# Performance work log

Hardware: AMD Instinct MI355X
Metric: run time of the kernel (lower is better)

The kernel has to match this reference:

```python
import jax, jax.numpy as jnp
import numpy as np

B, S, D = 4, 2048, 1024
NEG = -1e10

def setup_inputs() -> dict:
    key = jax.random.key(0)
    ks = jax.random.split(key, 8)
    scale = 1.0 / np.sqrt(D)
    return {
        "hidden_states": jax.random.normal(ks[0], (B, S, D), jnp.float32),
        "mask": jax.random.randint(ks[1], (B, S), 0, 2, jnp.int32),
        "Wq": jax.random.normal(ks[2], (D, D), jnp.float32) * scale,
        "bq": jnp.zeros((D,), jnp.float32),
        "Wk": jax.random.normal(ks[3], (D, D), jnp.float32) * scale,
        "bk": jnp.zeros((D,), jnp.float32),
        "Wv": jax.random.normal(ks[4], (D, D), jnp.float32) * scale,
        "bv": jnp.zeros((D,), jnp.float32),
        "Wo": jax.random.normal(ks[5], (D, D), jnp.float32) * scale,
        "bo": jnp.zeros((D,), jnp.float32),
    }

def reference(hidden_states, mask, Wq, bq, Wk, bk, Wv, bv, Wo, bo):
    # torch Linear: y = x @ W.T + b
    q = jnp.einsum('bsd,ed->bse', hidden_states, Wq) + bq
    k = jnp.einsum('bsd,ed->bse', hidden_states, Wk) + bk
    v = jnp.einsum('bsd,ed->bse', hidden_states, Wv) + bv
    inv_sqrt_d = jnp.asarray(int(hidden_states.shape[-1]) ** (-0.5), hidden_states.dtype)
    weight = jnp.einsum('bqd,bkd->bqk', q, k) * inv_sqrt_d  # [B,S,S]
    # mask viewed as [B,1,S]: key-padding mask broadcast over query dim
    m = mask.reshape(mask.shape[0], 1, mask.shape[1])
    weight = jnp.where(m == 0, jnp.asarray(NEG, weight.dtype), weight)
    a = jax.nn.softmax(weight, axis=-1)
    hid = jnp.einsum('bqk,bkd->bqd', a, v)
    hid_o = jnp.einsum('bsd,ed->bse', hid, Wo) + bo
    return hidden_states + hid_o  # residual=True
```

## Files before the change

### kernel.cpp

```cpp
#include <hip/hip_runtime.h>
#include <stdint.h>


typedef __attribute__((ext_vector_type(8))) short bf16x8;
typedef __attribute__((ext_vector_type(4))) float f32x4;

typedef __attribute__((address_space(3))) void lds_void_t;
typedef __attribute__((address_space(1))) const void glb_void_t;

__device__ __forceinline__ ushort f2bf(float f) {
  uint32_t u = __float_as_uint(f);
  u += 0x7FFF + ((u >> 16) & 1);
  return (ushort)(u >> 16);
}
__device__ __forceinline__ float bf2f(ushort u) {
  return __uint_as_float(((uint32_t)u) << 16);
}

__global__ __launch_bounds__(256) void convert_all(
    const float* __restrict__ X, const float* __restrict__ Wq,
    const float* __restrict__ Wk, const float* __restrict__ Wv,
    const float* __restrict__ Wo, const float* __restrict__ bq,
    const float* __restrict__ bk, const float* __restrict__ bv,
    ushort* __restrict__ Xb, ushort* __restrict__ Wqkvb,
    ushort* __restrict__ Wob, float* __restrict__ bqkv) {
  if (blockIdx.x >= 12288) {
#pragma unroll
    for (int u = 0; u < 3; ++u) {
      int base = (u * 256 + threadIdx.x) * 4;
      float4 v = (base < 1024)   ? *(const float4*)(bq + base)
               : (base < 2048)   ? *(const float4*)(bk + base - 1024)
                                 : *(const float4*)(bv + base - 2048);
      *(float4*)(bqkv + base) = v;
    }
    return;
  }
  int64_t o4 = ((int64_t)blockIdx.x * blockDim.x + threadIdx.x) * 4;
  const float* s; ushort* d; int64_t doff, soff;
  if (o4 < 8388608)        { s = X;  d = Xb;    doff = o4;            soff = o4; }
  else if (o4 < 9437184)   { s = Wq; d = Wqkvb; doff = o4 - 8388608;  soff = o4 - 8388608; }
  else if (o4 < 10485760)  { s = Wk; d = Wqkvb; doff = o4 - 8388608;  soff = o4 - 9437184; }
  else if (o4 < 11534336)  { s = Wv; d = Wqkvb; doff = o4 - 8388608;  soff = o4 - 10485760; }
  else                     { s = Wo; d = Wob;   doff = o4 - 11534336; soff = o4 - 11534336; }
  float4 v = *(const float4*)(s + soff);
  ushort4 o;
  o.x = f2bf(v.x); o.y = f2bf(v.y); o.z = f2bf(v.z); o.w = f2bf(v.w);
  *(ushort4*)(d + doff) = o;
}

#define BM 128
#define BKT 64

template <int MODE, int BNV>
__global__ __launch_bounds__(256) void gemm_bt(
    const ushort* __restrict__ Ag, const ushort* __restrict__ Bg,
    void* __restrict__ Og, const float* __restrict__ bias,
    const float* __restrict__ resid, ushort* __restrict__ Vt,
    const int* __restrict__ maskg, float* __restrict__ rowsum,
    int M, int N, int K, int lda, int ldb, int ldo,
    long long sAz, long long sBz, long long sOz, float scale) {
  constexpr int NFR = BNV / 32;
  __shared__ ushort LDSu[BM * BKT + BNV * BKT];
  ushort* const As = LDSu;
  ushort* const Bs = LDSu + BM * BKT;
  __shared__ int redn[4];

  const int z = blockIdx.z;
  const ushort* A = Ag + (int64_t)z * sAz;
  const ushort* B = Bg + (int64_t)z * sBz;

  const int tilesN = N / BNV;
  const int tm = blockIdx.x / tilesN;
  const int tn = blockIdx.x % tilesN;
  const int tid = threadIdx.x;
  const int wid = tid >> 6;
  const int lane = tid & 63;
  const int lr = lane & 15;
  const int kq = lane >> 4;
  const int wr = (wid >> 1) * 64;
  const int wc = (wid & 1) * (BNV / 2);

  if constexpr (MODE == 6) {
    const int4* mrow = (const int4*)(maskg + z * 2048);
    int4 ma = mrow[tid * 2];
    int4 mb = mrow[tid * 2 + 1];
    int cnt = (ma.x == 0) + (ma.y == 0) + (ma.z == 0) + (ma.w == 0) +
              (mb.x == 0) + (mb.y == 0) + (mb.z == 0) + (mb.w == 0);
#pragma unroll
    for (int off = 1; off < 64; off <<= 1) cnt += __shfl_xor(cnt, off);
    if (lane == 0) redn[wid] = cnt;
  }

  f32x4 acc[4][NFR];
#pragma unroll
  for (int m = 0; m < 4; ++m)
#pragma unroll
    for (int n = 0; n < NFR; ++n) acc[m][n] = (f32x4){0.f, 0.f, 0.f, 0.f};

  const int64_t abase = (int64_t)tm * BM;
  const int64_t bbase = (int64_t)tn * BNV;

  for (int kt = 0; kt < K; kt += BKT) {
    if (kt) __syncthreads();
#pragma unroll
    for (int r = 0; r < 4; ++r) {
      int idx = r * 256 + tid;
      int row = idx >> 3, slot = idx & 7;
      int sslot = slot ^ (row & 7);
      const ushort* ga = A + (abase + row) * lda + kt + sslot * 8;
      ushort* la = &As[(r * 256 + wid * 64) * 8];
      __builtin_amdgcn_global_load_lds((glb_void_t*)ga, (lds_void_t*)la, 16, 0, 0);
    }
#pragma unroll
    for (int r = 0; r < BNV / 32; ++r) {
      int idx = r * 256 + tid;
      int row = idx >> 3, slot = idx & 7;
      int sslot = slot ^ (row & 7);
      const ushort* gb = B + (bbase + row) * ldb + kt + sslot * 8;
      ushort* lb = &Bs[(r * 256 + wid * 64) * 8];
      __builtin_amdgcn_global_load_lds((glb_void_t*)gb, (lds_void_t*)lb, 16, 0, 0);
    }
    __syncthreads();

#pragma unroll
    for (int kk = 0; kk < 2; ++kk) {
      bf16x8 af[4], bfr[NFR];
#pragma unroll
      for (int m = 0; m < 4; ++m) {
        int row = wr + m * 16 + lr;
        int slot = (kk * 4 + kq) ^ (row & 7);
        af[m] = *(const bf16x8*)&As[row * 64 + slot * 8];
      }
#pragma unroll
      for (int n = 0; n < NFR; ++n) {
        int col = wc + n * 16 + lr;
        int slot = (kk * 4 + kq) ^ (col & 7);
        bfr[n] = *(const bf16x8*)&Bs[col * 64 + slot * 8];
      }
#pragma unroll
      for (int m = 0; m < 4; ++m)
#pragma unroll
        for (int n = 0; n < NFR; ++n)
          acc[m][n] = __builtin_amdgcn_mfma_f32_16x16x32_bf16(af[m], bfr[n], acc[m][n], 0, 0, 0);
    }
  }

  if constexpr (MODE == 5) {
    float part[4][4];
#pragma unroll
    for (int m = 0; m < 4; ++m)
#pragma unroll
      for (int i = 0; i < 4; ++i) part[m][i] = 0.f;
#pragma unroll
    for (int m = 0; m < 4; ++m) {
      int r0 = tm * BM + wr + m * 16 + kq * 4;
#pragma unroll
      for (int n = 0; n < NFR; ++n) {
        int c = tn * BNV + wc + n * 16 + lr;
#pragma unroll
        for (int i = 0; i < 4; ++i) {
          float e = __expf(acc[m][n][i]);
          ((ushort*)Og)[(int64_t)z * sOz + (int64_t)(r0 + i) * ldo + c] = f2bf(e);
          part[m][i] += e;
        }
      }
    }
#pragma unroll
    for (int off = 1; off <= 8; off <<= 1)
#pragma unroll
      for (int m = 0; m < 4; ++m)
#pragma unroll
        for (int i = 0; i < 4; ++i)
          part[m][i] += __shfl_xor(part[m][i], off);
    if (lr == 0) {
#pragma unroll
      for (int m = 0; m < 4; ++m)
#pragma unroll
        for (int i = 0; i < 4; ++i)
          atomicAdd(&rowsum[z * 2048 + tm * BM + wr + m * 16 + kq * 4 + i],
                    part[m][i]);
    }
  } else if constexpr (MODE == 6) {
    float nm = (float)(redn[0] + redn[1] + redn[2] + redn[3]);
    float invr[4][4];
#pragma unroll
    for (int m = 0; m < 4; ++m)
#pragma unroll
      for (int i = 0; i < 4; ++i)
        invr[m][i] =
            1.0f / (rowsum[z * 2048 + tm * BM + wr + m * 16 + kq * 4 + i] - nm);
#pragma unroll
    for (int m = 0; m < 4; ++m) {
      int r0 = tm * BM + wr + m * 16 + kq * 4;
#pragma unroll
      for (int n = 0; n < NFR; ++n) {
        int c = tn * BNV + wc + n * 16 + lr;
#pragma unroll
        for (int i = 0; i < 4; ++i)
          ((ushort*)Og)[(int64_t)z * sOz + (int64_t)(r0 + i) * ldo + c] =
              f2bf(acc[m][n][i] * invr[m][i]);
      }
    }
  } else if constexpr (MODE == 4) {
    if (tn < 8) {
#pragma unroll
      for (int m = 0; m < 4; ++m) {
        int r0 = tm * BM + wr + m * 16 + kq * 4;
#pragma unroll
        for (int n = 0; n < NFR; ++n) {
          int c = tn * BNV + wc + n * 16 + lr;
          const float bb = bias[c];
#pragma unroll
          for (int i = 0; i < 4; ++i)
            ((ushort*)Og)[(int64_t)(r0 + i) * 2048 + c] =
                f2bf((acc[m][n][i] + bb) * 0.03125f);
        }
      }
    } else if (tn < 16) {
#pragma unroll
      for (int m = 0; m < 4; ++m) {
        int r0 = tm * BM + wr + m * 16 + kq * 4;
        int4 mv = *(const int4*)(maskg + r0);
        int mk[4] = {mv.x, mv.y, mv.z, mv.w};
#pragma unroll
        for (int n = 0; n < NFR; ++n) {
          int c = tn * BNV + wc + n * 16 + lr;
          const float bb = bias[c];
#pragma unroll
          for (int i = 0; i < 4; ++i)
            ((ushort*)Og)[(int64_t)(r0 + i) * 2048 + c] =
                mk[i] ? f2bf(acc[m][n][i] + bb) : (ushort)0;
        }
      }
    } else {
      __syncthreads();
#pragma unroll
      for (int m = 0; m < 4; ++m) {
        int rl0 = wr + m * 16 + kq * 4;
        int4 mv = *(const int4*)(maskg + tm * BM + rl0);
        int mk[4] = {mv.x, mv.y, mv.z, mv.w};
#pragma unroll
        for (int n = 0; n < NFR; ++n) {
          int cl = wc + n * 16 + lr;
          const float bb = bias[tn * BNV + cl];
#pragma unroll
          for (int i = 0; i < 4; ++i) {
            int rl = rl0 + i;
            ushort v = mk[i] ? f2bf(acc[m][n][i] + bb) : (ushort)0;
            LDSu[cl * 128 + (rl ^ ((cl & 7) << 3))] = v;
          }
        }
      }
      __syncthreads();
      {
        const int e = tid >> 1, h = tid & 1;
        ushort* dst = Vt + (int64_t)((tn - 16) * BNV + e) * 8192 + tm * BM + h * 64;
        const ushort* src = &LDSu[e * 128 + h * 64];
#pragma unroll
        for (int g = 0; g < 8; ++g) {
          bf16x8 vv = *(const bf16x8*)&src[((g ^ (e & 7)) & 7) * 8];
          *(bf16x8*)&dst[g * 8] = vv;
        }
      }
    }
  } else {
#pragma unroll
    for (int m = 0; m < 4; ++m) {
      int r0 = tm * BM + wr + m * 16 + kq * 4;
#pragma unroll
      for (int n = 0; n < NFR; ++n) {
        int c = tn * BNV + wc + n * 16 + lr;
        const float bb = bias[c];
#pragma unroll
        for (int i = 0; i < 4; ++i) {
          int rrow = r0 + i;
          ((float*)Og)[(int64_t)rrow * ldo + c] =
              acc[m][n][i] + bb + resid[(int64_t)rrow * ldo + c];
        }
      }
    }
  }
}

extern "C" void kernel_launch(void* const* d_in, const int* in_sizes, int n_in,
                              void* d_out, int out_size, void* d_ws, size_t ws_size,
                              hipStream_t stream) {
  const float* hs = (const float*)d_in[0];
  const int* mask = (const int*)d_in[1];
  const float* Wq = (const float*)d_in[2];
  const float* bq = (const float*)d_in[3];
  const float* Wk = (const float*)d_in[4];
  const float* bk = (const float*)d_in[5];
  const float* Wv = (const float*)d_in[6];
  const float* bv = (const float*)d_in[7];
  const float* Wo = (const float*)d_in[8];
  const float* bo = (const float*)d_in[9];
  float* out = (float*)d_out;
  char* w = (char*)d_ws;

  ushort* Xb    = (ushort*)(w + 0);
  float*  rowsum = (float*)(w + 0);
  ushort* Wqkvb = (ushort*)(w + 16777216);
  ushort* Wob   = (ushort*)(w + 23068672);
  ushort* QKb   = (ushort*)(w + 25165824);
  ushort* Vt    = (ushort*)(w + 58720256);
  ushort* P     = (ushort*)(w + 75497472);
  float*  bqkv  = (float*)(w + 92274688);
  ushort* AO    = (ushort*)(w + 109051904);

  convert_all<<<12289, 256, 0, stream>>>(hs, Wq, Wk, Wv, Wo, bq, bk, bv,
                                         Xb, Wqkvb, Wob, bqkv);

  gemm_bt<4, 128><<<dim3(1536, 1, 1), 256, 0, stream>>>(Xb, Wqkvb, QKb, bqkv,
      nullptr, Vt, mask, nullptr,
      8192, 3072, 1024, 1024, 1024, 2048, 0, 0, 0, 1.f);

  hipMemsetAsync(rowsum, 0, 8192 * sizeof(float), stream);

  gemm_bt<5, 128><<<dim3(256, 1, 4), 256, 0, stream>>>(QKb, QKb + 1024, P,
      nullptr, nullptr, nullptr, nullptr, rowsum,
      2048, 2048, 1024, 2048, 2048, 2048,
      (long long)2048 * 2048, (long long)2048 * 2048, (long long)2048 * 2048,
      1.f);

  gemm_bt<6, 128><<<dim3(128, 1, 4), 256, 0, stream>>>(P, Vt, AO, nullptr,
      nullptr, nullptr, mask, rowsum,
      2048, 1024, 2048, 2048, 8192, 1024,
      (long long)2048 * 2048, (long long)2048, (long long)2048 * 1024, 1.f);

  gemm_bt<3, 64><<<dim3(1024, 1, 1), 256, 0, stream>>>(AO, Wob, (void*)out, bo,
      hs, nullptr, nullptr, nullptr,
      8192, 1024, 1024, 1024, 1024, 1024, 0, 0, 0, 1.f);
}
```

Baseline: 202.5 us.

## Compact masked keys and values to skip padded positions in attention

```diff
diff --git a/kernel.cpp b/kernel.cpp
--- a/kernel.cpp
+++ b/kernel.cpp
@@ -48,6 +48,43 @@
   *(ushort4*)(d + doff) = o;
 }
 
+__global__ __launch_bounds__(256) void compact_mask(const int* __restrict__ mask,
+                                                    int* __restrict__ meta) {
+  const int z = blockIdx.x;
+  const int* m = mask + z * 2048;
+  const int tid = threadIdx.x;
+  const int lane = tid & 63, wid = tid >> 6;
+  int4 a = ((const int4*)m)[tid * 2];
+  int4 b = ((const int4*)m)[tid * 2 + 1];
+  int v[8] = {a.x, a.y, a.z, a.w, b.x, b.y, b.z, b.w};
+  int s = 0;
+#pragma unroll
+  for (int j = 0; j < 8; ++j) s += v[j];
+  int incl = s;
+#pragma unroll
+  for (int off = 1; off < 64; off <<= 1) {
+    int t = __shfl_up(incl, off);
+    if (lane >= off) incl += t;
+  }
+  __shared__ int wtot[4];
+  if (lane == 63) wtot[wid] = incl;
+  __syncthreads();
+  int base = 0;
+#pragma unroll
+  for (int i = 0; i < 4; ++i)
+    if (i < wid) base += wtot[i];
+  int run = base + incl - s;
+#pragma unroll
+  for (int j = 0; j < 8; ++j) {
+    meta[z * 2048 + tid * 8 + j] = run;
+    run += v[j];
+  }
+  if (tid == 255) {
+    meta[8192 + z] = run;
+    meta[8196 + z] = (run + 63) & ~63;
+  }
+}
+
 #define BM 128
 #define BKT 64
 
@@ -56,22 +93,32 @@
     const ushort* __restrict__ Ag, const ushort* __restrict__ Bg,
     void* __restrict__ Og, const float* __restrict__ bias,
     const float* __restrict__ resid, ushort* __restrict__ Vt,
-    const int* __restrict__ maskg, float* __restrict__ rowsum,
+    const int* __restrict__ maskg, const int* __restrict__ meta,
+    float* __restrict__ rowsum,
     int M, int N, int K, int lda, int ldb, int ldo,
     long long sAz, long long sBz, long long sOz, float scale) {
   constexpr int NFR = BNV / 32;
   __shared__ ushort LDSu[BM * BKT + BNV * BKT];
   ushort* const As = LDSu;
   ushort* const Bs = LDSu + BM * BKT;
-  __shared__ int redn[4];
 
   const int z = blockIdx.z;
-  const ushort* A = Ag + (int64_t)z * sAz;
-  const ushort* B = Bg + (int64_t)z * sBz;
-
   const int tilesN = N / BNV;
   const int tm = blockIdx.x / tilesN;
   const int tn = blockIdx.x % tilesN;
+
+  int nkz = 0, nkpz = 0;
+  if constexpr (MODE == 5) {
+    nkz = meta[8192 + z];
+    nkpz = meta[8196 + z];
+    if (tn * BNV >= nkpz) return;
+  }
+  int Kloc = K;
+  if constexpr (MODE == 6) Kloc = meta[8196 + z];
+
+  const ushort* A = Ag + (int64_t)z * sAz;
+  const ushort* B = Bg + (int64_t)z * sBz;
+
   const int tid = threadIdx.x;
   const int wid = tid >> 6;
   const int lane = tid & 63;
@@ -80,17 +127,6 @@
   const int wr = (wid >> 1) * 64;
   const int wc = (wid & 1) * (BNV / 2);
 
-  if constexpr (MODE == 6) {
-    const int4* mrow = (const int4*)(maskg + z * 2048);
-    int4 ma = mrow[tid * 2];
-    int4 mb = mrow[tid * 2 + 1];
-    int cnt = (ma.x == 0) + (ma.y == 0) + (ma.z == 0) + (ma.w == 0) +
-              (mb.x == 0) + (mb.y == 0) + (mb.z == 0) + (mb.w == 0);
-#pragma unroll
-    for (int off = 1; off < 64; off <<= 1) cnt += __shfl_xor(cnt, off);
-    if (lane == 0) redn[wid] = cnt;
-  }
-
   f32x4 acc[4][NFR];
 #pragma unroll
   for (int m = 0; m < 4; ++m)
@@ -100,7 +136,7 @@
   const int64_t abase = (int64_t)tm * BM;
   const int64_t bbase = (int64_t)tn * BNV;
 
-  for (int kt = 0; kt < K; kt += BKT) {
+  for (int kt = 0; kt < Kloc; kt += BKT) {
     if (kt) __syncthreads();
 #pragma unroll
     for (int r = 0; r < 4; ++r) {
@@ -157,9 +193,10 @@
 #pragma unroll
       for (int n = 0; n < NFR; ++n) {
         int c = tn * BNV + wc + n * 16 + lr;
+        bool live = (c < nkz);
 #pragma unroll
         for (int i = 0; i < 4; ++i) {
-          float e = __expf(acc[m][n][i]);
+          float e = live ? __expf(acc[m][n][i]) : 0.f;
           ((ushort*)Og)[(int64_t)z * sOz + (int64_t)(r0 + i) * ldo + c] = f2bf(e);
           part[m][i] += e;
         }
@@ -181,14 +218,12 @@
                     part[m][i]);
     }
   } else if constexpr (MODE == 6) {
-    float nm = (float)(redn[0] + redn[1] + redn[2] + redn[3]);
     float invr[4][4];
 #pragma unroll
     for (int m = 0; m < 4; ++m)
 #pragma unroll
       for (int i = 0; i < 4; ++i)
-        invr[m][i] =
-            1.0f / (rowsum[z * 2048 + tm * BM + wr + m * 16 + kq * 4 + i] - nm);
+        invr[m][i] = 1.0f / rowsum[z * 2048 + tm * BM + wr + m * 16 + kq * 4 + i];
 #pragma unroll
     for (int m = 0; m < 4; ++m) {
       int r0 = tm * BM + wr + m * 16 + kq * 4;
@@ -212,24 +247,27 @@
           const float bb = bias[c];
 #pragma unroll
           for (int i = 0; i < 4; ++i)
-            ((ushort*)Og)[(int64_t)(r0 + i) * 2048 + c] =
+            ((ushort*)Og)[(int64_t)(r0 + i) * 1024 + c] =
                 f2bf((acc[m][n][i] + bb) * 0.03125f);
         }
       }
     } else if (tn < 16) {
+      ushort* Kc = (ushort*)Vt;
 #pragma unroll
       for (int m = 0; m < 4; ++m) {
         int r0 = tm * BM + wr + m * 16 + kq * 4;
+        int zb = r0 >> 11;
         int4 mv = *(const int4*)(maskg + r0);
         int mk[4] = {mv.x, mv.y, mv.z, mv.w};
+        int sl[4] = {meta[r0], meta[r0 + 1], meta[r0 + 2], meta[r0 + 3]};
 #pragma unroll
         for (int n = 0; n < NFR; ++n) {
-          int c = tn * BNV + wc + n * 16 + lr;
-          const float bb = bias[c];
+          int c = tn * BNV + wc + n * 16 + lr - 1024;
+          const float bb = bias[c + 1024];
 #pragma unroll
           for (int i = 0; i < 4; ++i)
-            ((ushort*)Og)[(int64_t)(r0 + i) * 2048 + c] =
-                mk[i] ? f2bf(acc[m][n][i] + bb) : (ushort)0;
+            if (mk[i])
+              Kc[(int64_t)(zb * 1280 + sl[i]) * 1024 + c] = f2bf(acc[m][n][i] + bb);
         }
       }
     } else {
@@ -237,8 +275,6 @@
 #pragma unroll
       for (int m = 0; m < 4; ++m) {
         int rl0 = wr + m * 16 + kq * 4;
-        int4 mv = *(const int4*)(maskg + tm * BM + rl0);
-        int mk[4] = {mv.x, mv.y, mv.z, mv.w};
 #pragma unroll
         for (int n = 0; n < NFR; ++n) {
           int cl = wc + n * 16 + lr;
@@ -246,20 +282,23 @@
 #pragma unroll
           for (int i = 0; i < 4; ++i) {
             int rl = rl0 + i;
-            ushort v = mk[i] ? f2bf(acc[m][n][i] + bb) : (ushort)0;
-            LDSu[cl * 128 + (rl ^ ((cl & 7) << 3))] = v;
+            LDSu[cl * 128 + (rl ^ ((cl & 7) << 3))] = f2bf(acc[m][n][i] + bb);
           }
         }
       }
       __syncthreads();
       {
         const int e = tid >> 1, h = tid & 1;
-        ushort* dst = Vt + (int64_t)((tn - 16) * BNV + e) * 8192 + tm * BM + h * 64;
-        const ushort* src = &LDSu[e * 128 + h * 64];
-#pragma unroll
-        for (int g = 0; g < 8; ++g) {
-          bf16x8 vv = *(const bf16x8*)&src[((g ^ (e & 7)) & 7) * 8];
-          *(bf16x8*)&dst[g * 8] = vv;
+        const int T0 = tm * BM + h * 64;
+        const int zb = tm >> 4;
+        ushort* vrow = ((ushort*)Vt) + 10485760 / 2
+                       + (int64_t)((tn - 16) * BNV + e) * 8192 + zb * 2048;
+        const ushort* src = &LDSu[e * 128];
+        const int sw = (e & 7) << 3;
+#pragma unroll 8
+        for (int j = 0; j < 64; ++j) {
+          int T = T0 + j;
+          if (maskg[T]) vrow[meta[T]] = src[(h * 64 + j) ^ sw];
         }
       }
     }
@@ -302,33 +341,39 @@
   float*  rowsum = (float*)(w + 0);
   ushort* Wqkvb = (ushort*)(w + 16777216);
   ushort* Wob   = (ushort*)(w + 23068672);
-  ushort* QKb   = (ushort*)(w + 25165824);
-  ushort* Vt    = (ushort*)(w + 58720256);
-  ushort* P     = (ushort*)(w + 75497472);
-  float*  bqkv  = (float*)(w + 92274688);
-  ushort* AO    = (ushort*)(w + 109051904);
+  int*    meta  = (int*)(w + 25165824);
+  float*  bqkv  = (float*)(w + 25165824 + 36864);
+  ushort* Qb    = (ushort*)(w + 25231360);
+  ushort* KcVtc = (ushort*)(w + 42008576);
+  ushort* Vtc   = (ushort*)(w + 52494336);
+  ushort* P     = (ushort*)(w + 69271552);
+  ushort* AO    = (ushort*)(w + 90243072);
 
   convert_all<<<12289, 256, 0, stream>>>(hs, Wq, Wk, Wv, Wo, bq, bk, bv,
                                          Xb, Wqkvb, Wob, bqkv);
 
-  gemm_bt<4, 128><<<dim3(1536, 1, 1), 256, 0, stream>>>(Xb, Wqkvb, QKb, bqkv,
-      nullptr, Vt, mask, nullptr,
-      8192, 3072, 1024, 1024, 1024, 2048, 0, 0, 0, 1.f);
+  compact_mask<<<4, 256, 0, stream>>>(mask, meta);
+
+  hipMemsetAsync(Vtc, 0, 16777216, stream);
+
+  gemm_bt<4, 128><<<dim3(1536, 1, 1), 256, 0, stream>>>(Xb, Wqkvb, Qb, bqkv,
+      nullptr, KcVtc, mask, meta, nullptr,
+      8192, 3072, 1024, 1024, 1024, 0, 0, 0, 0, 1.f);
 
   hipMemsetAsync(rowsum, 0, 8192 * sizeof(float), stream);
 
-  gemm_bt<5, 128><<<dim3(256, 1, 4), 256, 0, stream>>>(QKb, QKb + 1024, P,
-      nullptr, nullptr, nullptr, nullptr, rowsum,
-      2048, 2048, 1024, 2048, 2048, 2048,
-      (long long)2048 * 2048, (long long)2048 * 2048, (long long)2048 * 2048,
+  gemm_bt<5, 128><<<dim3(160, 1, 4), 256, 0, stream>>>(Qb, KcVtc, P,
+      nullptr, nullptr, nullptr, nullptr, meta, rowsum,
+      2048, 1280, 1024, 1024, 1024, 1280,
+      (long long)2048 * 1024, (long long)1280 * 1024, (long long)2048 * 1280,
       1.f);
 
-  gemm_bt<6, 128><<<dim3(128, 1, 4), 256, 0, stream>>>(P, Vt, AO, nullptr,
-      nullptr, nullptr, mask, rowsum,
-      2048, 1024, 2048, 2048, 8192, 1024,
-      (long long)2048 * 2048, (long long)2048, (long long)2048 * 1024, 1.f);
+  gemm_bt<6, 128><<<dim3(128, 1, 4), 256, 0, stream>>>(P, Vtc, AO, nullptr,
+      nullptr, nullptr, nullptr, meta, rowsum,
+      2048, 1024, 0, 1280, 8192, 1024,
+      (long long)2048 * 1280, (long long)2048, (long long)2048 * 1024, 1.f);
 
   gemm_bt<3, 64><<<dim3(1024, 1, 1), 256, 0, stream>>>(AO, Wob, (void*)out, bo,
-      hs, nullptr, nullptr, nullptr,
+      hs, nullptr, nullptr, nullptr, nullptr,
       8192, 1024, 1024, 1024, 1024, 1024, 0, 0, 0, 1.f);
 }
```

After: 227.4 us. 12.3% more time.
